# Performance work log

Measured on AMD Instinct MI355X. Metric: run time of the kernel, lower is better.

Reference implementation:

```python
import jax, jax.numpy as jnp
import numpy as np

LAM = 0.01   # sparsity_threshold -> softshrink lambda
EPS = 1e-8

def _ln(x, g, b):
    mu = jnp.mean(x, axis=-1, keepdims=True)
    var = jnp.mean((x - mu) ** 2, axis=-1, keepdims=True)
    return (x - mu) / jnp.sqrt(var + 1e-5) * g + b

def _cmatmul(xr, xi, w, b):
    # x: (B,H,W,nb,i)  w: (2,nb,i,o)  b: (2,nb,o)  -> complex block-diagonal matmul
    o_r = jnp.einsum('bhwni,nio->bhwno', xr, w[0]) - jnp.einsum('bhwni,nio->bhwno', xi, w[1]) + b[0]
    o_i = jnp.einsum('bhwni,nio->bhwno', xi, w[0]) + jnp.einsum('bhwni,nio->bhwno', xr, w[1]) + b[1]
    return o_r, o_i

def _softshrink(v):
    return jnp.where(v > LAM, v - LAM, jnp.where(v < -LAM, v + LAM, 0.0))

def _afno(xn, xp, w1, b1, w2, b2, w3, b3, alpha, H, W):
    # xn: (B,N,C_in) tokens, xp: (B,H,W,hid). layer_i == 0 path, num_blocks == 1.
    B, N, C = xn.shape
    hid = alpha.shape[-1]
    xf = jnp.fft.fft2(xn.reshape(B, H, W, C), axes=(1, 2), norm='ortho')
    xr = xf.real.reshape(B, H, W, 1, C)
    xi = xf.imag.reshape(B, H, W, 1, C)
    o1r, o1i = _cmatmul(xr, xi, w1, b1)           # (B,H,W,1,hid)
    xr = o1r.reshape(B, H, W, hid)
    xi = o1i.reshape(B, H, W, hid)
    pf = jnp.fft.fft2(xp, axes=(1, 2), norm='ortho')
    pr = pf.real.reshape(B, H, W, 1, hid)
    pi = pf.imag.reshape(B, H, W, 1, hid)
    tr, ti = _cmatmul(pr, pi, w3, b3)
    pr = tr.reshape(B, H, W, hid)
    pi = ti.reshape(B, H, W, hid)
    # Pangu-guided frequency modulation (real/imag component form)
    cross_r = pr * xr + pi * xi                   # Re(x_pangu * conj(x))
    mag_o = jnp.sqrt(xr ** 2 + xi ** 2)
    mag_p = jnp.sqrt(pr ** 2 + pi ** 2)
    phi_x = jnp.arctan2(xi, xr)
    phi_p = jnp.arctan2(pi, pr)
    sum_cos = alpha * jnp.cos(phi_x) + (1.0 - alpha) * jnp.cos(phi_p)
    sum_sin = alpha * jnp.sin(phi_x) + (1.0 - alpha) * jnp.sin(phi_p)
    nrm = jnp.sqrt(sum_cos ** 2 + sum_sin ** 2 + EPS)
    out_cos = sum_cos / nrm
    out_sin = sum_sin / nrm
    sim = cross_r / (mag_p * mag_o + EPS)
    soft = jax.nn.softmax(sim, axis=3)
    mag = mag_o * soft
    o1r = jax.nn.relu(mag * out_cos).reshape(B, H, W, 1, hid)
    o1i = jax.nn.relu(mag * out_sin).reshape(B, H, W, 1, hid)
    o2r, o2i = _cmatmul(o1r, o1i, w2, b2)
    o2r = _softshrink(o2r)
    o2i = _softshrink(o2i)
    xc = jax.lax.complex(o2r.reshape(B, H, W, hid), o2i.reshape(B, H, W, hid))
    y = jnp.fft.ifft2(xc, s=(H, W), axes=(1, 2), norm='ortho').real
    return y.reshape(B, N, hid)

def reference(x, x_pangu, z_fft, w1, b1, w2, b2, w3, b3, alpha,
              gamma1, beta1, gamma2, beta2, proj_w, proj_b,
              fc1_w, fc1_b, fc2_w, fc2_b):
    B, C, H, W = x.shape
    tok = x.reshape(B, C, H * W).transpose(0, 2, 1)      # (B,N,C_in)
    xp = x_pangu.transpose(0, 2, 3, 1)                   # (B,H,W,hid)
    residual = tok @ proj_w.T + proj_b                   # C_in != dim -> proj
    f = _afno(_ln(tok, gamma1, beta1), xp, w1, b1, w2, b2, w3, b3, alpha, H, W)
    h = f + residual                                     # double skip
    m = _ln(h, gamma2, beta2)
    m = jax.nn.gelu(m @ fc1_w.T + fc1_b, approximate=False) @ fc2_w.T + fc2_b
    out = m + h
    return out.reshape(B, H, W, -1).transpose(0, 3, 1, 2)

def setup_inputs():
    key = jax.random.key(0)
    ks = jax.random.split(key, 12)
    B, Cin, H, W = 8, 128, 64, 64
    hid, nb, mlp_hid = 256, 1, 2048
    s = 0.02
    return {
        'x': jax.random.normal(ks[0], (B, Cin, H, W), jnp.float32),
        'x_pangu': jax.random.normal(ks[1], (B, hid, H, W), jnp.float32),
        'z_fft': jax.random.normal(ks[2], (B, H, W, hid, 2), jnp.float32),
        'w1': s * jax.random.normal(ks[3], (2, nb, Cin, hid), jnp.float32),
        'b1': s * jax.random.normal(ks[4], (2, nb, hid), jnp.float32),
        'w2': s * jax.random.normal(ks[5], (2, nb, hid, hid), jnp.float32),
        'b2': s * jax.random.normal(ks[6], (2, nb, hid), jnp.float32),
        'w3': s * jax.random.normal(ks[7], (2, nb, hid, hid), jnp.float32),
        'b3': s * jax.random.normal(ks[8], (2, nb, hid), jnp.float32),
        'alpha': jnp.full((1, 1, 1, hid), 0.5, jnp.float32),
        'gamma1': jnp.ones((Cin,), jnp.float32),
        'beta1': jnp.zeros((Cin,), jnp.float32),
        'gamma2': jnp.ones((hid,), jnp.float32),
        'beta2': jnp.zeros((hid,), jnp.float32),
        'proj_w': s * jax.random.normal(ks[9], (hid, Cin), jnp.float32),
        'proj_b': jnp.zeros((hid,), jnp.float32),
        'fc1_w': s * jax.random.normal(ks[10], (mlp_hid, hid), jnp.float32),
        'fc1_b': jnp.zeros((mlp_hid,), jnp.float32),
        'fc2_w': s * jax.random.normal(ks[11], (hid, mlp_hid), jnp.float32),
        'fc2_b': jnp.zeros((hid,), jnp.float32),
    }
```

## Files before the change

kernel.cpp:

```cpp
#include <hip/hip_runtime.h>
#include <hip/hip_bf16.h>
#include <math.h>

#define NBATCH 8
#define HWP 4096
#define NTOK 32768
#define NTOKH 16896
#define CIN 128
#define HID 256
#define MLPH 2048
#define SLOTF 8388608L

typedef unsigned short u16;
typedef __attribute__((ext_vector_type(8))) short bf16x8;
typedef __attribute__((ext_vector_type(4))) float f32x4;
typedef __attribute__((ext_vector_type(8))) unsigned short ushort8_t;
typedef __attribute__((ext_vector_type(2))) unsigned long long u64x2;

__device__ __forceinline__ float bf2f(u16 v) { return __uint_as_float(((unsigned)v) << 16); }
__device__ __forceinline__ u16 f2bf(float f) {
    unsigned u = __float_as_uint(f);
    u = u + 0x7fffu + ((u >> 16) & 1u);
    return (u16)(u >> 16);
}
__device__ __forceinline__ u16 bits2bf(unsigned u) {
    u = u + 0x7fffu + ((u >> 16) & 1u);
    return (u16)(u >> 16);
}
__device__ __forceinline__ unsigned pk_bf16(float lo, float hi) {
    unsigned r;
    asm("v_cvt_pk_bf16_f32 %0, %1, %2" : "=v"(r) : "v"(lo), "v"(hi));
    return r;
}
__device__ __forceinline__ float sshrink(float v) {
    return v > 0.01f ? v - 0.01f : (v < -0.01f ? v + 0.01f : 0.f);
}
__device__ __forceinline__ float fast_gelu(float v) {
    float z = v * fmaf(0.0713548162726f, v * v, 1.59576912161f);
    float t = __builtin_amdgcn_exp2f(z * -1.44269504088896f);
    return v * __builtin_amdgcn_rcpf(1.f + t);
}

__global__ __launch_bounds__(256) void ln1_kernel(const float* __restrict__ x,
    const float* __restrict__ g, const float* __restrict__ be,
    float* __restrict__ xn, u16* __restrict__ xb)
{
    __shared__ float xt[CIN][65];
    __shared__ float mu_s[64], rs_s[64];
    int bid = blockIdx.x;
    int b = bid >> 6;
    int t0 = (bid & 63) << 6;
    int tid = threadIdx.x;
    for (int it = 0; it < 32; ++it) {
        int idx = (it << 8) + tid;
        int c = idx >> 6, t = idx & 63;
        xt[c][t] = x[(long)(b * CIN + c) * HWP + t0 + t];
    }
    __syncthreads();
    int tt = tid >> 2, p = tid & 3;
    float s = 0.f, ss = 0.f;
    #pragma unroll
    for (int i = 0; i < 32; ++i) {
        float v = xt[p * 32 + i][tt];
        s += v; ss += v * v;
    }
    s += __shfl_xor(s, 1); ss += __shfl_xor(ss, 1);
    s += __shfl_xor(s, 2); ss += __shfl_xor(ss, 2);
    if (p == 0) {
        float mu = s * (1.f / CIN);
        float var = ss * (1.f / CIN) - mu * mu;
        mu_s[tt] = mu;
        rs_s[tt] = rsqrtf(var + 1e-5f);
    }
    __syncthreads();
    for (int it = 0; it < 32; ++it) {
        int idx = (it << 8) + tid;
        int t = idx >> 7, c = idx & 127;
        xn[((long)b * HWP + t0 + t) * CIN + c] = (xt[c][t] - mu_s[t]) * rs_s[t] * g[c] + be[c];
    }
    #pragma unroll
    for (int it = 0; it < 8; ++it) {
        int idx = (it << 8) + tid;
        int t = idx >> 5, c4 = (idx & 31) << 2;
        uint2 pk;
        pk.x = pk_bf16(xt[c4 + 0][t], xt[c4 + 1][t]);
        pk.y = pk_bf16(xt[c4 + 2][t], xt[c4 + 3][t]);
        *(uint2*)&xb[((long)b * HWP + t0 + t) * CIN + c4] = pk;
    }
}

__device__ __forceinline__ void wcvt_body(const float* __restrict__ w, int K,
    u16* __restrict__ out, int idx)
{
    int k = idx >> 8, o = idx & 255;
    float w0 = w[k * 256 + o];
    float w1v = w[K * 256 + k * 256 + o];
    long K2 = 2L * K;
    out[(long)o * K2 + k] = f2bf(w0);
    out[(long)o * K2 + K + k] = f2bf(-w1v);
    out[(long)(256 + o) * K2 + k] = f2bf(w1v);
    out[(long)(256 + o) * K2 + K + k] = f2bf(w0);
}
__device__ __forceinline__ void f2bf_body(const float* __restrict__ in,
    u16* __restrict__ out, int i)
{
    float4 v = *(const float4*)&in[i];
    ushort4 o;
    o.x = f2bf(v.x); o.y = f2bf(v.y); o.z = f2bf(v.z); o.w = f2bf(v.w);
    *(ushort4*)&out[i] = o;
}
__global__ __launch_bounds__(256) void setup_kernel(
    const float* __restrict__ w1, const float* __restrict__ w3,
    const float* __restrict__ w2, const float* __restrict__ fc1w,
    const float* __restrict__ fc2w, const float* __restrict__ pw,
    u16* __restrict__ TWB, u16* __restrict__ W1c, u16* __restrict__ W3c,
    u16* __restrict__ W2c, u16* __restrict__ WB1, u16* __restrict__ WB2,
    u16* __restrict__ PWB)
{
    int bid = blockIdx.x, tid = threadIdx.x;
    if (bid < 64) {
        int idx = bid * 256 + tid;
        int n = idx >> 7, kcol = idx & 127;
        int j = kcol & 63, p = kcol >> 6;
        int np = n & 63, q = n >> 6;
        float th = 6.283185307179586f * (float)((j * np) & 63) / 64.f;
        float sv, cv;
        sincosf(th, &sv, &cv);
        float fw = (q == 0) ? (p == 0 ? cv : sv) : (p == 0 ? -sv : cv);
        float iv = (q == 0) ? (p == 0 ? cv : -sv) : (p == 0 ? sv : cv);
        fw *= 0.125f; iv *= 0.125f;
        u16 fh = f2bf(fw), ih = f2bf(iv);
        TWB[idx] = fh;
        TWB[16384 + idx] = f2bf(fw - bf2f(fh));
        TWB[32768 + idx] = ih;
        TWB[49152 + idx] = f2bf(iv - bf2f(ih));
    } else if (bid < 192) {
        wcvt_body(w1, 128, W1c, (bid - 64) * 256 + tid);
    } else if (bid < 448) {
        wcvt_body(w3, 256, W3c, (bid - 192) * 256 + tid);
    } else if (bid < 704) {
        wcvt_body(w2, 256, W2c, (bid - 448) * 256 + tid);
    } else if (bid < 1216) {
        f2bf_body(fc1w, WB1, ((bid - 704) * 256 + tid) * 4);
    } else if (bid < 1728) {
        f2bf_body(fc2w, WB2, ((bid - 1216) * 256 + tid) * 4);
    } else {
        f2bf_body(pw, PWB, ((bid - 1728) * 256 + tid) * 4);
    }
}

template<int INMODE, int REALOUT, int NT, int USELO>
__global__ __launch_bounds__(256) void dftm_kernel(
    const void* __restrict__ inp, const u16* __restrict__ tw,
    void* __restrict__ outp, const float* __restrict__ addend,
    int nch, long IB, long IK, long IC, long JS, long PS,
    long OB, long OK, long OC, long KS, long PS2, int kmax)
{
    constexpr int K = (INMODE == 1) ? 128 : 64;
    constexpr int AST = (K == 128) ? 136 : 72;
    constexpr int MFR = REALOUT ? 2 : 4;
    __shared__ __align__(16) u16 smem[128 * 136];
    int tid = threadIdx.x;
    int lane = tid & 63;
    int bid = blockIdx.x;
    int b = bid / (64 * nch);
    int rem = bid % (64 * nch);
    int keep = rem / nch;
    int ch = rem % nch;
    long ibase = b * IB + keep * IK + ch * IC;
    long obase = b * OB + keep * OK + ch * OC;

    if (INMODE == 0) {
        const float* inF = (const float*)inp;
        #pragma unroll
        for (int it = 0; it < 8; ++it) {
            int idx = (it << 8) + tid;
            int j = idx >> 5, c4 = (idx & 31) << 2;
            u64x2 v = *(const u64x2*)(inF + ibase + (long)j * JS + c4);
            #pragma unroll
            for (int i = 0; i < 4; ++i) {
                int vv = (i + lane) & 3;
                unsigned long long q = (vv & 2) ? v.y : v.x;
                unsigned fb = (unsigned)(q >> ((vv & 1) << 5));
                smem[(c4 + vv) * AST + j] = bits2bf(fb);
            }
        }
    } else if (INMODE == 1) {
        const u16* inU = (const u16*)inp;
        #pragma unroll
        for (int it = 0; it < 8; ++it) {
            int idx = (it << 8) + tid;
            int run = idx >> 4, c8 = (idx & 15) << 3;
            int j = run >> 1, p = run & 1;
            u64x2 v = *(const u64x2*)(inU + ibase + (long)j * JS + (long)p * PS + c8);
            int col = p * 64 + j;
            #pragma unroll
            for (int i = 0; i < 8; ++i) {
                int vv = (i + lane) & 7;
                unsigned long long q = (vv & 4) ? v.y : v.x;
                u16 val = (u16)(q >> ((vv & 3) << 4));
                smem[(c8 + vv) * AST + col] = val;
            }
        }
    } else {
        const float* inF = (const float*)inp;
        #pragma unroll
        for (int it = 0; it < 8; ++it) {
            int idx = (it << 8) + tid;
            int row = idx >> 4, j4 = (idx & 15) << 2;
            u64x2 v = *(const u64x2*)(inF + ibase + (long)row * JS + j4);
            ushort4 o;
            o.x = bits2bf((unsigned)v.x);
            o.y = bits2bf((unsigned)(v.x >> 32));
            o.z = bits2bf((unsigned)v.y);
            o.w = bits2bf((unsigned)(v.y >> 32));
            *(ushort4*)&smem[row * AST + j4] = o;
        }
    }
    __syncthreads();

    int w = tid >> 6;
    int ln15 = lane & 15, kg = lane >> 4;
    int wrow = REALOUT ? (w << 5) : ((w >> 1) << 6);
    int wcol = REALOUT ? 0 : ((w & 1) << 6);
    f32x4 acc[MFR][NT] = {};
    #pragma unroll
    for (int kk = 0; kk < K / 32; ++kk) {
        bf16x8 av[MFR];
        #pragma unroll
        for (int m = 0; m < MFR; ++m)
            av[m] = *(const bf16x8*)&smem[(wrow + m * 16 + ln15) * AST + kk * 32 + kg * 8];
        #pragma unroll
        for (int n = 0; n < NT; ++n) {
            const u16* tb = tw + (wcol + n * 16 + ln15) * 128 + kk * 32 + kg * 8;
            bf16x8 bh = *(const bf16x8*)tb;
            #pragma unroll
            for (int m = 0; m < MFR; ++m)
                acc[m][n] = __builtin_amdgcn_mfma_f32_16x16x32_bf16(av[m], bh, acc[m][n], 0, 0, 0);
            if (USELO) {
                bf16x8 bl = *(const bf16x8*)(tb + 16384);
                #pragma unroll
                for (int m = 0; m < MFR; ++m)
                    acc[m][n] = __builtin_amdgcn_mfma_f32_16x16x32_bf16(av[m], bl, acc[m][n], 0, 0, 0);
            }
        }
    }
    __syncthreads();

    if (REALOUT == 0) {
        #pragma unroll
        for (int m = 0; m < MFR; ++m)
            #pragma unroll
            for (int n = 0; n < NT; ++n) {
                int base = (wcol + n * 16 + ln15) * 136 + wrow + m * 16 + kg * 4;
                uint2 pk;
                pk.x = pk_bf16(acc[m][n][0], acc[m][n][1]);
                pk.y = pk_bf16(acc[m][n][2], acc[m][n][3]);
                *(uint2*)&smem[base] = pk;
            }
        __syncthreads();
        u16* outU = (u16*)outp;
        #pragma unroll
        for (int it = 0; it < 8; ++it) {
            int idx = (it << 8) + tid;
            int n = idx >> 4, c8 = (idx & 15) << 3;
            int k = n & 63, p = n >> 6;
            if (k <= kmax)
                *(ushort8_t*)&outU[obase + (long)k * KS + (long)p * PS2 + c8] =
                    *(const ushort8_t*)&smem[n * 136 + c8];
        }
    } else {
        float* ef = (float*)smem;
        #pragma unroll
        for (int m = 0; m < MFR; ++m)
            #pragma unroll
            for (int n = 0; n < NT; ++n) {
                float4 vv = make_float4(acc[m][n][0], acc[m][n][1], acc[m][n][2], acc[m][n][3]);
                *(float4*)&ef[(n * 16 + ln15) * 132 + wrow + m * 16 + kg * 4] = vv;
            }
        __syncthreads();
        float* outF = (float*)outp;
        #pragma unroll
        for (int it = 0; it < 8; ++it) {
            int idx = (it << 8) + tid;
            int k = idx >> 5, c4 = (idx & 31) << 2;
            long a = obase + (long)k * KS + c4;
            float4 v = *(const float4*)&ef[k * 132 + c4];
            float4 rv = *(const float4*)&addend[a];
            v.x += rv.x; v.y += rv.y; v.z += rv.z; v.w += rv.w;
            *(float4*)&outF[a] = v;
        }
    }
}

__global__ __launch_bounds__(256) void mod_kernel(
    const u16* __restrict__ x1, const u16* __restrict__ p3,
    const float* __restrict__ alpha, u16* __restrict__ a2)
{
    int tid = threadIdx.x;
    int lane = tid & 63;
    int wv = tid >> 6;
    int tp = blockIdx.x * 4 + wv;
    int b = tp / 2112;
    int r = tp - b * 2112;
    int kh = r >> 6, kw = r & 63;
    long ibase = (long)tp * 512 + lane * 4;
    ushort4 xr4 = *(const ushort4*)&x1[ibase];
    ushort4 xi4 = *(const ushort4*)&x1[ibase + 256];
    ushort4 pr4 = *(const ushort4*)&p3[ibase];
    ushort4 pi4 = *(const ushort4*)&p3[ibase + 256];
    float4 al4 = *(const float4*)&alpha[lane * 4];
    u16 xru[4] = {xr4.x, xr4.y, xr4.z, xr4.w};
    u16 xiu[4] = {xi4.x, xi4.y, xi4.z, xi4.w};
    u16 pru[4] = {pr4.x, pr4.y, pr4.z, pr4.w};
    u16 piu[4] = {pi4.x, pi4.y, pi4.z, pi4.w};
    float alv[4] = {al4.x, al4.y, al4.z, al4.w};
    float mo[4], oc[4], os[4], sim[4];
    #pragma unroll
    for (int q = 0; q < 4; ++q) {
        float xr = bf2f(xru[q]), xi = bf2f(xiu[q]);
        float pr = bf2f(pru[q]), pi = bf2f(piu[q]);
        float al = alv[q];
        float m = __builtin_amdgcn_sqrtf(xr * xr + xi * xi);
        float mp = __builtin_amdgcn_sqrtf(pr * pr + pi * pi);
        float cx, sx, cp, sp;
        if (m > 0.f) { float rr = __builtin_amdgcn_rcpf(m); cx = xr * rr; sx = xi * rr; }
        else { cx = 1.f; sx = 0.f; }
        if (mp > 0.f) { float rr = __builtin_amdgcn_rcpf(mp); cp = pr * rr; sp = pi * rr; }
        else { cp = 1.f; sp = 0.f; }
        float sc = al * cx + (1.f - al) * cp;
        float ssn = al * sx + (1.f - al) * sp;
        float rn = __builtin_amdgcn_rsqf(sc * sc + ssn * ssn + 1e-8f);
        mo[q] = m;
        oc[q] = sc * rn;
        os[q] = ssn * rn;
        float cross = pr * xr + pi * xi;
        sim[q] = cross * __builtin_amdgcn_rcpf(mp * m + 1e-8f);
    }
    float mv = fmaxf(fmaxf(sim[0], sim[1]), fmaxf(sim[2], sim[3]));
    #pragma unroll
    for (int off = 1; off < 64; off <<= 1) mv = fmaxf(mv, __shfl_xor(mv, off));
    float e[4];
    float sum = 0.f;
    #pragma unroll
    for (int q = 0; q < 4; ++q) {
        e[q] = __builtin_amdgcn_exp2f((sim[q] - mv) * 1.44269504088896f);
        sum += e[q];
    }
    #pragma unroll
    for (int off = 1; off < 64; off <<= 1) sum += __shfl_xor(sum, off);
    float rs = __builtin_amdgcn_rcpf(sum);
    float orf[4], ipf[4], imf[4];
    #pragma unroll
    for (int q = 0; q < 4; ++q) {
        float mag = mo[q] * e[q] * rs;
        orf[q] = fmaxf(mag * oc[q], 0.f);
        ipf[q] = fmaxf(mag * os[q], 0.f);
        imf[q] = fmaxf(-mag * os[q], 0.f);
    }
    uint2 o_r, o_ip, o_im;
    o_r.x = pk_bf16(orf[0], orf[1]);  o_r.y = pk_bf16(orf[2], orf[3]);
    o_ip.x = pk_bf16(ipf[0], ipf[1]); o_ip.y = pk_bf16(ipf[2], ipf[3]);
    o_im.x = pk_bf16(imf[0], imf[1]); o_im.y = pk_bf16(imf[2], imf[3]);
    long pbase = ((long)b * 4096 + kh * 64 + kw) * 512 + lane * 4;
    *(uint2*)&a2[pbase] = o_r;
    *(uint2*)&a2[pbase + 256] = o_ip;
    if (kh >= 1 && kh <= 31) {
        long mbase = ((long)b * 4096 + (64 - kh) * 64 + ((64 - kw) & 63)) * 512 + lane * 4;
        *(uint2*)&a2[mbase] = o_r;
        *(uint2*)&a2[mbase + 256] = o_im;
    }
}

__global__ __launch_bounds__(256) void ln2_kernel(const float* __restrict__ h,
    const float* __restrict__ g, const float* __restrict__ be, u16* __restrict__ m)
{
    int t = blockIdx.x, c = threadIdx.x;
    float v = h[(long)t * HID + c];
    float s = v, ss = v * v;
    #pragma unroll
    for (int off = 1; off < 64; off <<= 1) { s += __shfl_xor(s, off); ss += __shfl_xor(ss, off); }
    __shared__ float r1[4], r2[4];
    int wid = c >> 6;
    if ((c & 63) == 0) { r1[wid] = s; r2[wid] = ss; }
    __syncthreads();
    s = r1[0] + r1[1] + r1[2] + r1[3];
    ss = r2[0] + r2[1] + r2[2] + r2[3];
    float mu = s * (1.f / HID);
    float var = ss * (1.f / HID) - mu * mu;
    float rstd = rsqrtf(var + 1e-5f);
    m[(long)t * HID + c] = f2bf((v - mu) * rstd * g[c] + be[c]);
}

template<int EPI, int BK>
__global__ __launch_bounds__(256) void gemm_mfma_kernel(
    const u16* __restrict__ A, const u16* __restrict__ Bw,
    const float* __restrict__ bias, const float* __restrict__ hbuf,
    void* __restrict__ outp, int M, int N, int K)
{
    constexpr bool SWAP = (EPI == 0 || EPI == 2 || EPI == 4);
    __shared__ __align__(16) char smem[(EPI == 1 || EPI == 5) ? (128 * 132 * 4) : (128 * 136 * 2)];
    u16* ldsA = (u16*)smem;
    u16* ldsB = (u16*)(smem + 128 * BK * 2);
    int tid = threadIdx.x;
    int nbn = N >> 7;
    int cpx = (int)gridDim.x >> 3;
    int bid = ((int)blockIdx.x & 7) * cpx + ((int)blockIdx.x >> 3);
    int bRow = (bid / nbn) << 7;
    int bCol = (bid % nbn) << 7;
    int lane = tid & 63;
    int w = tid >> 6;
    int wr = (w >> 1) << 6;
    int wc = (w & 1) << 6;
    int ln15 = lane & 15;
    int kg = lane >> 4;

    f32x4 acc[4][4] = {};

    constexpr int GR = BK / 8;
    int srow = tid / GR;
    int sg = tid % GR;
    int gsg = sg ^ (srow & 7);
    const u16* gA = A + (long)(bRow + srow) * K + gsg * 8;
    const u16* gB = Bw + (long)(bCol + srow) * K + gsg * 8;
    u16* lA = ldsA + srow * BK + sg * 8;
    u16* lB = ldsB + srow * BK + sg * 8;
    constexpr int RPR = 256 / GR;
    constexpr int NCH = 128 / RPR;

    for (int k0 = 0; k0 < K; k0 += BK) {
        __syncthreads();
        #pragma unroll
        for (int c = 0; c < NCH; ++c) {
            __builtin_amdgcn_global_load_lds(
                (const __attribute__((address_space(1))) void*)(gA + (long)c * RPR * K + k0),
                (__attribute__((address_space(3))) void*)(lA + c * RPR * BK), 16, 0, 0);
            __builtin_amdgcn_global_load_lds(
                (const __attribute__((address_space(1))) void*)(gB + (long)c * RPR * K + k0),
                (__attribute__((address_space(3))) void*)(lB + c * RPR * BK), 16, 0, 0);
        }
        __syncthreads();
        #pragma unroll
        for (int kk = 0; kk < BK; kk += 32) {
            int gbase = (kk >> 3) + kg;
            bf16x8 av[4], bv[4];
            #pragma unroll
            for (int m = 0; m < 4; ++m) {
                int row = wr + m * 16 + ln15;
                av[m] = *(const bf16x8*)(ldsA + row * BK + ((gbase ^ (row & 7)) << 3));
            }
            #pragma unroll
            for (int n = 0; n < 4; ++n) {
                int row = wc + n * 16 + ln15;
                bv[n] = *(const bf16x8*)(ldsB + row * BK + ((gbase ^ (row & 7)) << 3));
            }
            #pragma unroll
            for (int m = 0; m < 4; ++m)
                #pragma unroll
                for (int n = 0; n < 4; ++n) {
                    if (SWAP)
                        acc[m][n] = __builtin_amdgcn_mfma_f32_16x16x32_bf16(bv[n], av[m], acc[m][n], 0, 0, 0);
                    else
                        acc[m][n] = __builtin_amdgcn_mfma_f32_16x16x32_bf16(av[m], bv[n], acc[m][n], 0, 0, 0);
                }
        }
    }
    __syncthreads();

    if (EPI == 0 || EPI == 2 || EPI == 4) {
        u16* lds2 = (u16*)smem;
        #pragma unroll
        for (int n = 0; n < 4; ++n) {
            float4 bn4 = *(const float4*)&bias[bCol + wc + n * 16 + kg * 4];
            #pragma unroll
            for (int m = 0; m < 4; ++m) {
                float v0 = acc[m][n][0] + bn4.x;
                float v1 = acc[m][n][1] + bn4.y;
                float v2 = acc[m][n][2] + bn4.z;
                float v3 = acc[m][n][3] + bn4.w;
                if (EPI == 0) { v0 = fast_gelu(v0); v1 = fast_gelu(v1); v2 = fast_gelu(v2); v3 = fast_gelu(v3); }
                if (EPI == 4) { v0 = sshrink(v0); v1 = sshrink(v1); v2 = sshrink(v2); v3 = sshrink(v3); }
                uint2 pk;
                pk.x = pk_bf16(v0, v1);
                pk.y = pk_bf16(v2, v3);
                int tokenLocal = wr + m * 16 + ln15;
                int nLocal = wc + n * 16 + kg * 4;
                *(uint2*)&lds2[tokenLocal * 136 + nLocal] = pk;
            }
        }
        __syncthreads();
        u16* O = (u16*)outp;
        #pragma unroll
        for (int it = 0; it < 8; ++it) {
            int idx = (it << 8) + tid;
            int row = idx >> 4, c8 = (idx & 15) << 3;
            *(ushort8_t*)&O[(long)(bRow + row) * N + bCol + c8] = *(const ushort8_t*)&lds2[row * 136 + c8];
        }
    } else if (EPI == 5) {
        float* ldsf = (float*)smem;
        float bn[4];
        #pragma unroll
        for (int n = 0; n < 4; ++n) bn[n] = bias[bCol + wc + n * 16 + ln15];
        #pragma unroll
        for (int m = 0; m < 4; ++m)
            #pragma unroll
            for (int n = 0; n < 4; ++n) {
                int col = wc + n * 16 + ln15;
                #pragma unroll
                for (int r = 0; r < 4; ++r) {
                    int row = wr + m * 16 + kg * 4 + r;
                    ldsf[row * 132 + col] = acc[m][n][r] + bn[n];
                }
            }
        __syncthreads();
        float* O = (float*)outp;
        #pragma unroll
        for (int it = 0; it < 16; ++it) {
            int idx = (it << 8) + tid;
            int row = idx >> 5, c4 = (idx & 31) << 2;
            *(float4*)&O[(long)(bRow + row) * N + bCol + c4] = *(const float4*)&ldsf[row * 132 + c4];
        }
    } else {
        float* ldsf = (float*)smem;
        float bn[4];
        #pragma unroll
        for (int n = 0; n < 4; ++n) bn[n] = bias[bCol + wc + n * 16 + ln15];
        #pragma unroll
        for (int m = 0; m < 4; ++m)
            #pragma unroll
            for (int n = 0; n < 4; ++n) {
                int col = wc + n * 16 + ln15;
                float4 vv;
                #pragma unroll
                for (int r = 0; r < 4; ++r) {
                    int row = wr + m * 16 + kg * 4 + r;
                    float v = acc[m][n][r] + bn[n] + hbuf[(long)(bRow + row) * HID + bCol + col];
                    ((float*)&vv)[r] = v;
                }
                *(float4*)&ldsf[col * 132 + wr + m * 16 + kg * 4] = vv;
            }
        __syncthreads();
        float* O = (float*)outp;
        int b = bRow >> 12;
        int s0 = bRow & 4095;
        #pragma unroll
        for (int it = 0; it < 16; ++it) {
            int idx = (it << 8) + tid;
            int oc = idx >> 5, r4 = (idx & 31) << 2;
            *(float4*)&O[((long)(b * HID + bCol + oc)) * HWP + s0 + r4] = *(const float4*)&ldsf[oc * 132 + r4];
        }
    }
}

extern "C" void kernel_launch(void* const* d_in, const int* in_sizes, int n_in,
                              void* d_out, int out_size, void* d_ws, size_t ws_size,
                              hipStream_t stream)
{
    (void)in_sizes; (void)n_in; (void)out_size; (void)ws_size;
    const float* x     = (const float*)d_in[0];
    const float* xp    = (const float*)d_in[1];
    const float* w1    = (const float*)d_in[3];
    const float* b1    = (const float*)d_in[4];
    const float* w2    = (const float*)d_in[5];
    const float* b2    = (const float*)d_in[6];
    const float* w3    = (const float*)d_in[7];
    const float* b3    = (const float*)d_in[8];
    const float* alpha = (const float*)d_in[9];
    const float* g1    = (const float*)d_in[10];
    const float* be1   = (const float*)d_in[11];
    const float* g2    = (const float*)d_in[12];
    const float* be2   = (const float*)d_in[13];
    const float* pw    = (const float*)d_in[14];
    const float* pb    = (const float*)d_in[15];
    const float* fc1w  = (const float*)d_in[16];
    const float* fc1b  = (const float*)d_in[17];
    const float* fc2w  = (const float*)d_in[18];
    const float* fc2b  = (const float*)d_in[19];
    float* out = (float*)d_out;

    float* ws = (float*)d_ws;
    float* S0 = ws + 0 * SLOTF;
    float* S1 = ws + 1 * SLOTF;
    float* S2 = ws + 2 * SLOTF;
    float* S3 = ws + 3 * SLOTF;
    float* S4 = ws + 4 * SLOTF;
    float* S5 = ws + 5 * SLOTF;
    float* S6 = ws + 6 * SLOTF;

    float* RES  = S0;
    float* XN   = S1;
    u16*   M1x  = (u16*)S2;
    u16*   XF   = (u16*)S3;
    u16*   X1   = (u16*)S4;
    u16*   M1p  = (u16*)S2;
    u16*   PF   = (u16*)S3;
    u16*   P3   = (u16*)S5;
    u16*   A2   = (u16*)S2;
    u16*   O2b  = (u16*)S3;
    u16*   M2   = (u16*)S2;
    float* Hb   = S6;
    u16*   Mb16 = (u16*)S1;
    u16*   HIDB = (u16*)S2;

    u16* TWB  = (u16*)(S1 + SLOTF / 2);
    u16* TW_F = TWB;
    u16* TW_I = TWB + 32768;
    u16* W1c  = TWB + 65536;
    u16* W3c  = W1c + 131072;
    u16* W2c  = W3c + 262144;
    u16* WB1  = W2c + 262144;
    u16* WB2  = WB1 + 524288;
    u16* PWB  = WB2 + 524288;
    u16* XB   = TWB + 2097152;

    dim3 blk(256);

    setup_kernel<<<1760, blk, 0, stream>>>(w1, w3, w2, fc1w, fc2w, pw,
        TWB, W1c, W3c, W2c, WB1, WB2, PWB);

    ln1_kernel<<<512, blk, 0, stream>>>(x, g1, be1, XN, XB);
    gemm_mfma_kernel<5, 128><<<512, blk, 0, stream>>>(XB, PWB, pb, nullptr,
        (void*)RES, NTOK, HID, CIN);

    dftm_kernel<0, 0, 4, 0><<<512, blk, 0, stream>>>(XN, TW_F, M1x, nullptr,
        1, 524288L, 8192L, 0L, 128L, 0L, 1048576L, 16384L, 0L, 128L, 8192L, 63);
    dftm_kernel<1, 0, 3, 0><<<512, blk, 0, stream>>>(M1x, TW_F, XF, nullptr,
        1, 1048576L, 128L, 0L, 16384L, 8192L, 540672L, 256L, 0L, 16384L, 128L, 32);
    gemm_mfma_kernel<2, 64><<<528, blk, 0, stream>>>(XF, W1c, b1, nullptr,
        (void*)X1, NTOKH, 512, 256);

    dftm_kernel<2, 0, 4, 0><<<1024, blk, 0, stream>>>(xp, TW_F, M1p, nullptr,
        2, 1048576L, 64L, 524288L, 4096L, 0L, 2097152L, 32768L, 128L, 256L, 16384L, 63);
    dftm_kernel<1, 0, 3, 0><<<1024, blk, 0, stream>>>(M1p, TW_F, PF, nullptr,
        2, 2097152L, 256L, 128L, 32768L, 16384L, 1081344L, 512L, 128L, 32768L, 256L, 32);
    gemm_mfma_kernel<2, 64><<<528, blk, 0, stream>>>(PF, W3c, b3, nullptr,
        (void*)P3, NTOKH, 512, 512);

    mod_kernel<<<4224, blk, 0, stream>>>(X1, P3, alpha, A2);
    gemm_mfma_kernel<4, 64><<<1024, blk, 0, stream>>>(A2, W2c, b2, nullptr,
        (void*)O2b, NTOK, 512, 512);

    dftm_kernel<1, 0, 4, 0><<<1024, blk, 0, stream>>>(O2b, TW_I, M2, nullptr,
        2, 2097152L, 512L, 128L, 32768L, 256L, 2097152L, 256L, 128L, 32768L, 16384L, 63);
    dftm_kernel<1, 1, 4, 1><<<1024, blk, 0, stream>>>(M2, TW_I, Hb, RES,
        2, 2097152L, 32768L, 128L, 256L, 16384L, 1048576L, 16384L, 128L, 256L, 0L, 63);

    ln2_kernel<<<32768, blk, 0, stream>>>(Hb, g2, be2, Mb16);
    gemm_mfma_kernel<0, 64><<<4096, blk, 0, stream>>>(Mb16, WB1, fc1b, nullptr,
        (void*)HIDB, NTOK, MLPH, HID);
    gemm_mfma_kernel<1, 128><<<512, blk, 0, stream>>>(HIDB, WB2, fc2b, Hb,
        (void*)out, NTOK, HID, MLPH);
}
```

Baseline: 334.3 us.

## Fuse MLP fc1, GELU and fc2 into one kernel keeping hidden activations on-chip

Replaces the two MLP GEMM launches with a single kernel. Each block holds a 64-token tile of normalized activations in LDS and walks the 2048-wide hidden dimension in chunks of 32. For each chunk it computes fc1 plus GELU, stages the result in LDS as bf16, and accumulates fc2 into registers. This removes the global write and re-read of the 32768x2048 bf16 hidden tensor. In exchange, W1 and W2 are streamed again by every block, there are two barriers per chunk, and the launch has only 512 blocks with a 64-token tile and 16 accumulator fragments per thread, which may limit occupancy and overlap.

```diff
diff --git a/kernel.cpp b/kernel.cpp
--- a/kernel.cpp
+++ b/kernel.cpp
@@ -552,6 +552,125 @@
     }
 }
 
+__global__ __launch_bounds__(256) void mlp_fused2_kernel(
+    const u16* __restrict__ A,
+    const u16* __restrict__ W1,
+    const u16* __restrict__ W2,
+    const float* __restrict__ b1,
+    const float* __restrict__ b2,
+    const float* __restrict__ hbuf,
+    float* __restrict__ out)
+{
+    __shared__ __align__(16) u16 sA[64 * 256];
+    __shared__ __align__(16) u16 sW1[32 * 256];
+    __shared__ __align__(16) u16 sW2[256 * 32];
+    __shared__ __align__(16) u16 sH[64 * 32];
+    int tid = threadIdx.x;
+    int lane = tid & 63;
+    int wv = tid >> 6;
+    int tw = wv << 4;
+    int ln15 = lane & 15, kg = lane >> 4;
+    int bRow = (int)blockIdx.x << 6;
+    int tok = tw + ln15;
+
+    #pragma unroll
+    for (int r = 0; r < 8; ++r) {
+        int row = r * 8 + (tid >> 5);
+        int sg = tid & 31;
+        int gsg = sg ^ (row & 7);
+        __builtin_amdgcn_global_load_lds(
+            (const __attribute__((address_space(1))) void*)(A + (long)(bRow + row) * 256 + gsg * 8),
+            (__attribute__((address_space(3))) void*)(sA + row * 256 + sg * 8), 16, 0, 0);
+    }
+
+    f32x4 acc2[16] = {};
+
+    for (int c = 0; c < 64; ++c) {
+        __syncthreads();
+        #pragma unroll
+        for (int r = 0; r < 4; ++r) {
+            int row = r * 8 + (tid >> 5);
+            int sg = tid & 31;
+            int gsg = sg ^ (row & 7);
+            __builtin_amdgcn_global_load_lds(
+                (const __attribute__((address_space(1))) void*)(W1 + (long)(c * 32 + row) * 256 + gsg * 8),
+                (__attribute__((address_space(3))) void*)(sW1 + row * 256 + sg * 8), 16, 0, 0);
+        }
+        #pragma unroll
+        for (int r = 0; r < 4; ++r) {
+            int row = r * 64 + (tid >> 2);
+            int sg = tid & 3;
+            int gsg = sg ^ (row & 3);
+            __builtin_amdgcn_global_load_lds(
+                (const __attribute__((address_space(1))) void*)(W2 + (long)row * 2048 + c * 32 + gsg * 8),
+                (__attribute__((address_space(3))) void*)(sW2 + row * 32 + sg * 8), 16, 0, 0);
+        }
+        __syncthreads();
+
+        f32x4 acc1[2] = {};
+        #pragma unroll
+        for (int ks = 0; ks < 8; ++ks) {
+            int gfull = ks * 4 + kg;
+            bf16x8 av = *(const bf16x8*)(sA + tok * 256 + ((gfull ^ (tok & 7)) << 3));
+            #pragma unroll
+            for (int n = 0; n < 2; ++n) {
+                int row_h = n * 16 + ln15;
+                bf16x8 bv = *(const bf16x8*)(sW1 + row_h * 256 + ((gfull ^ (row_h & 7)) << 3));
+                acc1[n] = __builtin_amdgcn_mfma_f32_16x16x32_bf16(bv, av, acc1[n], 0, 0, 0);
+            }
+        }
+        #pragma unroll
+        for (int n = 0; n < 2; ++n) {
+            float4 bn4 = *(const float4*)&b1[c * 32 + n * 16 + kg * 4];
+            float v0 = fast_gelu(acc1[n][0] + bn4.x);
+            float v1 = fast_gelu(acc1[n][1] + bn4.y);
+            float v2 = fast_gelu(acc1[n][2] + bn4.z);
+            float v3 = fast_gelu(acc1[n][3] + bn4.w);
+            uint2 pk;
+            pk.x = pk_bf16(v0, v1);
+            pk.y = pk_bf16(v2, v3);
+            int gi = 2 * n + (kg >> 1);
+            *(uint2*)&sH[tok * 32 + ((gi ^ (tok & 3)) << 3) + ((kg & 1) << 2)] = pk;
+        }
+        bf16x8 av2 = *(const bf16x8*)(sH + tok * 32 + ((kg ^ (tok & 3)) << 3));
+        #pragma unroll
+        for (int n = 0; n < 16; ++n) {
+            int row_o = n * 16 + ln15;
+            bf16x8 bv2 = *(const bf16x8*)(sW2 + row_o * 32 + ((kg ^ (row_o & 3)) << 3));
+            acc2[n] = __builtin_amdgcn_mfma_f32_16x16x32_bf16(av2, bv2, acc2[n], 0, 0, 0);
+        }
+    }
+
+    float* ef = (float*)sA;
+    int b = bRow >> 12;
+    int s0 = bRow & 4095;
+    #pragma unroll
+    for (int oc = 0; oc < 4; ++oc) {
+        __syncthreads();
+        #pragma unroll
+        for (int nn = 0; nn < 4; ++nn) {
+            int n = oc * 4 + nn;
+            int o = n * 16 + ln15;
+            float bb = b2[o];
+            float4 vv;
+            #pragma unroll
+            for (int r = 0; r < 4; ++r) {
+                int tokr = tw + kg * 4 + r;
+                ((float*)&vv)[r] = acc2[n][r] + bb + hbuf[(long)(bRow + tokr) * 256 + o];
+            }
+            *(float4*)&ef[(o - oc * 64) * 68 + tw + kg * 4] = vv;
+        }
+        __syncthreads();
+        #pragma unroll
+        for (int it = 0; it < 4; ++it) {
+            int idx = (it << 8) + tid;
+            int ol = idx >> 4, t4 = (idx & 15) << 2;
+            *(float4*)&out[((long)(b * 256 + oc * 64 + ol)) * 4096 + s0 + t4] =
+                *(const float4*)&ef[ol * 68 + t4];
+        }
+    }
+}
+
 extern "C" void kernel_launch(void* const* d_in, const int* in_sizes, int n_in,
                               void* d_out, int out_size, void* d_ws, size_t ws_size,
                               hipStream_t stream)
@@ -600,7 +719,6 @@
     u16*   M2   = (u16*)S2;
     float* Hb   = S6;
     u16*   Mb16 = (u16*)S1;
-    u16*   HIDB = (u16*)S2;
 
     u16* TWB  = (u16*)(S1 + SLOTF / 2);
     u16* TW_F = TWB;
@@ -646,8 +764,5 @@
         2, 2097152L, 32768L, 128L, 256L, 16384L, 1048576L, 16384L, 128L, 256L, 0L, 63);
 
     ln2_kernel<<<32768, blk, 0, stream>>>(Hb, g2, be2, Mb16);
-    gemm_mfma_kernel<0, 64><<<4096, blk, 0, stream>>>(Mb16, WB1, fc1b, nullptr,
-        (void*)HIDB, NTOK, MLPH, HID);
-    gemm_mfma_kernel<1, 128><<<512, blk, 0, stream>>>(HIDB, WB2, fc2b, Hb,
-        (void*)out, NTOK, HID, MLPH);
-}
+    mlp_fused2_kernel<<<512, blk, 0, stream>>>(Mb16, WB1, WB2, fc1b, fc2b, Hb, out);
+}
```

Measured after the change: 343.9 us. +2.9%, slower.
